# Performance work log

Hardware: AMD Instinct MI355X
Metric: run time of the kernel (lower is better)

The kernel has to match this reference:

```python
import jax, jax.numpy as jnp
import numpy as np

B, S, HID = 2, 2048, 4096
NH, NKV, HD = 32, 8, 128
G = 128  # quant group size along input dim
NEG_INF = -1e9


def _rope_tables(key):
    inv_freq = 1.0 / (10000.0 ** (jnp.arange(0, HD, 2, dtype=jnp.float32) / HD))  # [HD/2]
    pos = jnp.arange(S, dtype=jnp.float32)
    ang = pos[:, None] * inv_freq[None, :]                  # [S, HD/2]
    emb = jnp.concatenate([ang, ang], axis=-1)              # [S, HD]
    cos = jnp.broadcast_to(jnp.cos(emb)[None], (B, S, HD))
    sin = jnp.broadcast_to(jnp.sin(emb)[None], (B, S, HD))
    return cos, sin


def setup_inputs() -> dict:
    key = jax.random.key(0)
    ks = jax.random.split(key, 10)
    hidden_states = jax.random.normal(ks[0], (B, S, HID), dtype=jnp.float32)
    cos, sin = _rope_tables(ks[1])
    causal = jnp.tril(jnp.ones((S, S), dtype=bool))
    attention_mask = jnp.broadcast_to(
        jnp.where(causal, 0.0, NEG_INF).astype(jnp.float32)[None, None], (B, 1, S, S))

    def qlinear(k, out_dim, in_dim):
        k1, k2 = jax.random.split(k)
        qw = jax.random.randint(k1, (out_dim, in_dim), 0, 16, dtype=jnp.int32)
        scale = jax.random.uniform(k2, (out_dim, in_dim // G), dtype=jnp.float32) * 0.01 + 0.001
        return qw, scale

    q_qw, q_scale = qlinear(ks[2], NH * HD, HID)
    k_qw, k_scale = qlinear(ks[3], NKV * HD, HID)
    v_qw, v_scale = qlinear(ks[4], NKV * HD, HID)
    o_qw, o_scale = qlinear(ks[5], HID, NH * HD)
    return dict(hidden_states=hidden_states, cos=cos, sin=sin,
                attention_mask=attention_mask,
                q_qw=q_qw, q_scale=q_scale, k_qw=k_qw, k_scale=k_scale,
                v_qw=v_qw, v_scale=v_scale, o_qw=o_qw, o_scale=o_scale)


def _dequant(qw, scale):
    # int4 codes in [0,16), zero-point 8, per-(row, input-group) scale
    out_dim, in_dim = qw.shape
    w = (qw.astype(jnp.float32) - 8.0).reshape(out_dim, in_dim // G, G)
    return (w * scale[:, :, None]).reshape(out_dim, in_dim)


def _rotate_half(x):
    x1, x2 = jnp.split(x, 2, axis=-1)
    return jnp.concatenate([-x2, x1], axis=-1)


def reference(hidden_states, cos, sin, attention_mask,
              q_qw, q_scale, k_qw, k_scale, v_qw, v_scale, o_qw, o_scale):
    scaling = HD ** -0.5
    Wq = _dequant(q_qw, q_scale)
    Wk = _dequant(k_qw, k_scale)
    Wv = _dequant(v_qw, v_scale)
    Wo = _dequant(o_qw, o_scale)

    q = jnp.einsum('bsh,oh->bso', hidden_states, Wq).reshape(B, S, NH, HD).transpose(0, 2, 1, 3)
    k = jnp.einsum('bsh,oh->bso', hidden_states, Wk).reshape(B, S, NKV, HD).transpose(0, 2, 1, 3)
    v = jnp.einsum('bsh,oh->bso', hidden_states, Wv).reshape(B, S, NKV, HD).transpose(0, 2, 1, 3)

    c = cos[:, None, :, :]  # [B,1,S,HD]
    s = sin[:, None, :, :]
    q = q * c + _rotate_half(q) * s
    k = k * c + _rotate_half(k) * s

    groups = NH // NKV
    k = jnp.repeat(k, groups, axis=1)  # [B,NH,S,HD]
    v = jnp.repeat(v, groups, axis=1)

    scores = jnp.einsum('bhsd,bhtd->bhst', q, k) * scaling + attention_mask
    probs = jax.nn.softmax(scores, axis=-1)
    ctx = jnp.einsum('bhst,bhtd->bhsd', probs, v)        # [B,NH,S,HD]
    ctx = ctx.transpose(0, 2, 1, 3).reshape(B, S, NH * HD)
    return jnp.einsum('bso,ho->bsh', ctx, Wo.T) if False else jnp.einsum('bsi,oi->bso', ctx, Wo)
```

## Files before the change

### kernel.cpp

```cpp
#include <hip/hip_runtime.h>
#include <hip/hip_bf16.h>

#define B_ 2
#define S_ 2048
#define HID_ 4096
#define NH_ 32
#define NKV_ 8
#define HD_ 128
#define T_ (B_*S_)

typedef __bf16 bf16;
typedef __bf16 bf16x8 __attribute__((ext_vector_type(8)));
typedef __bf16 bf16x4 __attribute__((ext_vector_type(4)));
typedef float f32x4 __attribute__((ext_vector_type(4)));

__device__ __forceinline__ void load_lds16(const void* g, void* l) {
  __builtin_amdgcn_global_load_lds((const __attribute__((address_space(1))) void*)g,
                                   (__attribute__((address_space(3))) void*)l, 16, 0, 0);
}

#define DPP_ROR(x, n) __int_as_float(__builtin_amdgcn_update_dpp( \
    __float_as_int(x), __float_as_int(x), 0x120 | (n), 0xf, 0xf, false))
__device__ __forceinline__ float red16_max(float x) {
  x = fmaxf(x, DPP_ROR(x, 1)); x = fmaxf(x, DPP_ROR(x, 2));
  x = fmaxf(x, DPP_ROR(x, 4)); x = fmaxf(x, DPP_ROR(x, 8));
  return x;
}
__device__ __forceinline__ float red16_sum(float x) {
  x += DPP_ROR(x, 1); x += DPP_ROR(x, 2);
  x += DPP_ROR(x, 4); x += DPP_ROR(x, 8);
  return x;
}

__global__ __launch_bounds__(256) void cvt_bf16_kernel(const float* __restrict__ in,
                                                       bf16* __restrict__ out, int n4) {
  int idx = blockIdx.x * 256 + threadIdx.x;
  if (idx >= n4) return;
  float4 v = ((const float4*)in)[idx];
  bf16x4 o;
  o.x = (bf16)v.x; o.y = (bf16)v.y; o.z = (bf16)v.z; o.w = (bf16)v.w;
  ((bf16x4*)out)[idx] = o;
}

__global__ __launch_bounds__(256) void dequant_kernel(const int* __restrict__ qw,
                                                      const float* __restrict__ scale,
                                                      bf16* __restrict__ out,
                                                      int OD, int ID) {
  int idx = blockIdx.x * 256 + threadIdx.x;
  int perRow = ID >> 3;
  int total = OD * perRow;
  if (idx >= total) return;
  int o = idx / perRow;
  int ic = idx - o * perRow;
  float s = scale[o * (ID >> 7) + ((ic * 8) >> 7)];
  const int* q = qw + (size_t)o * ID + ic * 8;
  int4 q0 = *(const int4*)q;
  int4 q1 = *(const int4*)(q + 4);
  bf16x8 r;
  r[0] = (bf16)((q0.x - 8) * s);
  r[1] = (bf16)((q0.y - 8) * s);
  r[2] = (bf16)((q0.z - 8) * s);
  r[3] = (bf16)((q0.w - 8) * s);
  r[4] = (bf16)((q1.x - 8) * s);
  r[5] = (bf16)((q1.y - 8) * s);
  r[6] = (bf16)((q1.z - 8) * s);
  r[7] = (bf16)((q1.w - 8) * s);
  *(bf16x8*)(out + (size_t)o * ID + ic * 8) = r;
}

__global__ __launch_bounds__(256) void gemm_bt_kernel(const bf16* __restrict__ A,
                                                      const bf16* __restrict__ Bm,
                                                      void* __restrict__ Cout,
                                                      int N, int K, int c_fp32) {
  __shared__ bf16 As[8192];
  __shared__ bf16 Bs[8192];
  int tid = threadIdx.x;
  int wave = tid >> 6, lane = tid & 63, quad = lane >> 4, l16 = lane & 15;
  int m0 = blockIdx.y * 128, n0 = blockIdx.x * 128;
  int wm = (wave >> 1) * 64, wn = (wave & 1) * 64;

  int srow = lane >> 3;
  int schunk = (lane & 7) ^ (srow & 7);
  const bf16* Ab[4];
  const bf16* Bb[4];
#pragma unroll
  for (int u = 0; u < 4; u++) {
    int t = wave + 4 * u;
    Ab[u] = A  + (size_t)(m0 + 8 * t + srow) * K + schunk * 8;
    Bb[u] = Bm + (size_t)(n0 + 8 * t + srow) * K + schunk * 8;
  }

  f32x4 acc[4][4];
#pragma unroll
  for (int mt = 0; mt < 4; mt++)
#pragma unroll
    for (int nt = 0; nt < 4; nt++) acc[mt][nt] = (f32x4){0.f, 0.f, 0.f, 0.f};

  for (int k0 = 0; k0 < K; k0 += 64) {
    __syncthreads();
#pragma unroll
    for (int u = 0; u < 4; u++) {
      int t = wave + 4 * u;
      load_lds16(Ab[u] + k0, (char*)As + t * 1024);
      load_lds16(Bb[u] + k0, (char*)Bs + t * 1024);
    }
    __syncthreads();
#pragma unroll
    for (int kk = 0; kk < 2; kk++) {
      bf16x8 af[4], bfr[4];
#pragma unroll
      for (int mt = 0; mt < 4; mt++) {
        int r = wm + mt * 16 + l16;
        af[mt] = *(const bf16x8*)((const char*)As + r * 128 + (((kk * 4 + quad) ^ (r & 7)) << 4));
      }
#pragma unroll
      for (int nt = 0; nt < 4; nt++) {
        int r = wn + nt * 16 + l16;
        bfr[nt] = *(const bf16x8*)((const char*)Bs + r * 128 + (((kk * 4 + quad) ^ (r & 7)) << 4));
      }
#pragma unroll
      for (int mt = 0; mt < 4; mt++)
#pragma unroll
        for (int nt = 0; nt < 4; nt++)
          acc[mt][nt] = __builtin_amdgcn_mfma_f32_16x16x32_bf16(af[mt], bfr[nt], acc[mt][nt], 0, 0, 0);
    }
  }

#pragma unroll
  for (int mt = 0; mt < 4; mt++)
#pragma unroll
    for (int nt = 0; nt < 4; nt++)
#pragma unroll
      for (int r = 0; r < 4; r++) {
        int rr = m0 + wm + mt * 16 + quad * 4 + r;
        int cc = n0 + wn + nt * 16 + l16;
        if (c_fp32) ((float*)Cout)[(size_t)rr * N + cc] = acc[mt][nt][r];
        else        ((bf16*)Cout)[(size_t)rr * N + cc] = (bf16)acc[mt][nt][r];
      }
}

__global__ __launch_bounds__(256) void gemm_rope_kernel(const bf16* __restrict__ A,
                                                        const bf16* __restrict__ Bm,
                                                        bf16* __restrict__ Out,
                                                        int N, int K,
                                                        const float* __restrict__ cosT,
                                                        const float* __restrict__ sinT,
                                                        float outscale) {
  __shared__ char smem[32768];
  bf16* As = (bf16*)smem;
  bf16* Bs = (bf16*)(smem + 16384);
  float* Ex = (float*)smem;
  int tid = threadIdx.x;
  int wave = tid >> 6, lane = tid & 63, quad = lane >> 4, l16 = lane & 15;
  int m0 = blockIdx.y * 128, n0 = blockIdx.x * 128;
  int wm = (wave >> 1) * 64, wn = (wave & 1) * 64;

  int srow = lane >> 3;
  int schunk = (lane & 7) ^ (srow & 7);
  const bf16* Ab[4];
  const bf16* Bb[4];
#pragma unroll
  for (int u = 0; u < 4; u++) {
    int t = wave + 4 * u;
    Ab[u] = A  + (size_t)(m0 + 8 * t + srow) * K + schunk * 8;
    Bb[u] = Bm + (size_t)(n0 + 8 * t + srow) * K + schunk * 8;
  }

  f32x4 acc[4][4];
#pragma unroll
  for (int mt = 0; mt < 4; mt++)
#pragma unroll
    for (int nt = 0; nt < 4; nt++) acc[mt][nt] = (f32x4){0.f, 0.f, 0.f, 0.f};

  for (int k0 = 0; k0 < K; k0 += 64) {
    __syncthreads();
#pragma unroll
    for (int u = 0; u < 4; u++) {
      int t = wave + 4 * u;
      load_lds16(Ab[u] + k0, (char*)As + t * 1024);
      load_lds16(Bb[u] + k0, (char*)Bs + t * 1024);
    }
    __syncthreads();
#pragma unroll
    for (int kk = 0; kk < 2; kk++) {
      bf16x8 af[4], bfr[4];
#pragma unroll
      for (int mt = 0; mt < 4; mt++) {
        int r = wm + mt * 16 + l16;
        af[mt] = *(const bf16x8*)((const char*)As + r * 128 + (((kk * 4 + quad) ^ (r & 7)) << 4));
      }
#pragma unroll
      for (int nt = 0; nt < 4; nt++) {
        int r = wn + nt * 16 + l16;
        bfr[nt] = *(const bf16x8*)((const char*)Bs + r * 128 + (((kk * 4 + quad) ^ (r & 7)) << 4));
      }
#pragma unroll
      for (int mt = 0; mt < 4; mt++)
#pragma unroll
        for (int nt = 0; nt < 4; nt++)
          acc[mt][nt] = __builtin_amdgcn_mfma_f32_16x16x32_bf16(af[mt], bfr[nt], acc[mt][nt], 0, 0, 0);
    }
  }

  int myb = tid * 17;
  int pb = (tid ^ 64) * 17;
#pragma unroll
  for (int mt = 0; mt < 4; mt++) {
    __syncthreads();
#pragma unroll
    for (int nt = 0; nt < 4; nt++)
#pragma unroll
      for (int r = 0; r < 4; r++)
        Ex[myb + nt * 4 + r] = acc[mt][nt][r];
    __syncthreads();
    int rowb = m0 + wm + mt * 16 + quad * 4;
#pragma unroll
    for (int nt = 0; nt < 4; nt++) {
      int cc = n0 + wn + nt * 16 + l16;
      int d = cc & 127;
#pragma unroll
      for (int r = 0; r < 4; r++) {
        int row = rowb + r;
        int t = row & (S_ - 1);
        float self = acc[mt][nt][r];
        float other = Ex[pb + nt * 4 + r];
        float c = cosT[t * 128 + d], s = sinT[t * 128 + d];
        float o = (d < 64) ? (self * c - other * s) : (self * c + other * s);
        Out[(size_t)row * N + cc] = (bf16)(o * outscale);
      }
    }
  }
}

template<int FUSE_ROPE, int C_FP32>
__global__ __launch_bounds__(512, 2) void gemm256_kernel(const bf16* __restrict__ A,
                                                         const bf16* __restrict__ Bm,
                                                         void* __restrict__ Cout,
                                                         int N, int K,
                                                         const float* __restrict__ cosT,
                                                         const float* __restrict__ sinT,
                                                         float outscale) {
  __shared__ char smem[131072];
  const int tid = threadIdx.x;
  const int wave = tid >> 6, lane = tid & 63, quad = lane >> 4, l16 = lane & 15;
  const int wm = (wave >> 2) * 128, wn = (wave & 3) * 64;

  int bid = blockIdx.y * gridDim.x + blockIdx.x;
  int cpx = (gridDim.x * gridDim.y) >> 3;
  int wgid = (bid & 7) * cpx + (bid >> 3);
  int m0 = (wgid / gridDim.x) * 256;
  int n0 = (wgid % gridDim.x) * 256;

  const int srow = wave * 16 + (lane >> 2);
  const int sc = (lane & 3) ^ ((lane >> 2) & 3) ^ quad;
  const bf16* aS0 = A  + (size_t)(m0 + srow) * K + sc * 8;
  const bf16* aS1 = A  + (size_t)(m0 + 128 + srow) * K + sc * 8;
  const bf16* bS0 = Bm + (size_t)(n0 + srow) * K + sc * 8;
  const bf16* bS1 = Bm + (size_t)(n0 + 128 + srow) * K + sc * 8;
  const int wl = wave * 1024;

  const int rslot = ((quad ^ (l16 & 3) ^ ((l16 >> 2) & 3)) << 4);
  const int aoff = (wm + l16) * 64 + rslot;
  const int boff = (wn + l16) * 64 + rslot;

  f32x4 acc[8][4];
#pragma unroll
  for (int mt = 0; mt < 8; mt++)
#pragma unroll
    for (int nt = 0; nt < 4; nt++) acc[mt][nt] = (f32x4){0.f, 0.f, 0.f, 0.f};

  load_lds16(aS0,      smem +     0 + wl); load_lds16(aS1,      smem +  8192 + wl);
  load_lds16(bS0,      smem + 32768 + wl); load_lds16(bS1,      smem + 40960 + wl);
  load_lds16(aS0 + 32, smem + 16384 + wl); load_lds16(aS1 + 32, smem + 24576 + wl);
  load_lds16(bS0 + 32, smem + 49152 + wl); load_lds16(bS1 + 32, smem + 57344 + wl);
  asm volatile("s_waitcnt vmcnt(0)" ::: "memory");
  __builtin_amdgcn_s_barrier();

  const int NT = K >> 6;
  for (int t = 0; t < NT; ++t) {
    const char* base = smem + (t & 1) * 65536;
    char* nb = smem + ((t & 1) ^ 1) * 65536;
    const int off = (t + 1) << 6;
    const bool more = (t + 1) < NT;
    bf16x8 afA[4], afB[4], bfr[4];

#pragma unroll
    for (int i = 0; i < 4; i++) afA[i] = *(const bf16x8*)(base + aoff + i * 1024);
#pragma unroll
    for (int i = 0; i < 4; i++) bfr[i] = *(const bf16x8*)(base + 32768 + boff + i * 1024);
    if (more) { load_lds16(aS0 + off, nb + wl); load_lds16(aS1 + off, nb + 8192 + wl); }
    __builtin_amdgcn_s_barrier();
    __builtin_amdgcn_s_setprio(1);
#pragma unroll
    for (int mt = 0; mt < 4; mt++)
#pragma unroll
      for (int nt = 0; nt < 4; nt++)
        acc[mt][nt] = __builtin_amdgcn_mfma_f32_16x16x32_bf16(afA[mt], bfr[nt], acc[mt][nt], 0, 0, 0);
    __builtin_amdgcn_s_setprio(0);
    __builtin_amdgcn_s_barrier();

#pragma unroll
    for (int i = 0; i < 4; i++) afB[i] = *(const bf16x8*)(base + aoff + (i + 4) * 1024);
    if (more) { load_lds16(bS0 + off, nb + 32768 + wl); load_lds16(bS1 + off, nb + 40960 + wl); }
    if (t == NT - 1) asm volatile("s_waitcnt vmcnt(0)" ::: "memory");
    else             asm volatile("s_waitcnt vmcnt(4)" ::: "memory");
    __builtin_amdgcn_s_barrier();
    __builtin_amdgcn_s_setprio(1);
#pragma unroll
    for (int mt = 0; mt < 4; mt++)
#pragma unroll
      for (int nt = 0; nt < 4; nt++)
        acc[mt + 4][nt] = __builtin_amdgcn_mfma_f32_16x16x32_bf16(afB[mt], bfr[nt], acc[mt + 4][nt], 0, 0, 0);
    __builtin_amdgcn_s_setprio(0);
    __builtin_amdgcn_s_barrier();

#pragma unroll
    for (int i = 0; i < 4; i++) afA[i] = *(const bf16x8*)(base + 16384 + aoff + i * 1024);
#pragma unroll
    for (int i = 0; i < 4; i++) bfr[i] = *(const bf16x8*)(base + 49152 + boff + i * 1024);
    if (more) { load_lds16(aS0 + off + 32, nb + 16384 + wl); load_lds16(aS1 + off + 32, nb + 24576 + wl); }
    __builtin_amdgcn_s_barrier();
    __builtin_amdgcn_s_setprio(1);
#pragma unroll
    for (int mt = 0; mt < 4; mt++)
#pragma unroll
      for (int nt = 0; nt < 4; nt++)
        acc[mt][nt] = __builtin_amdgcn_mfma_f32_16x16x32_bf16(afA[mt], bfr[nt], acc[mt][nt], 0, 0, 0);
    __builtin_amdgcn_s_setprio(0);
    __builtin_amdgcn_s_barrier();

#pragma unroll
    for (int i = 0; i < 4; i++) afB[i] = *(const bf16x8*)(base + 16384 + aoff + (i + 4) * 1024);
    if (more) {
      load_lds16(bS0 + off + 32, nb + 49152 + wl); load_lds16(bS1 + off + 32, nb + 57344 + wl);
      asm volatile("s_waitcnt vmcnt(4)" ::: "memory");
    }
    __builtin_amdgcn_s_barrier();
    __builtin_amdgcn_s_setprio(1);
#pragma unroll
    for (int mt = 0; mt < 4; mt++)
#pragma unroll
      for (int nt = 0; nt < 4; nt++)
        acc[mt + 4][nt] = __builtin_amdgcn_mfma_f32_16x16x32_bf16(afB[mt], bfr[nt], acc[mt + 4][nt], 0, 0, 0);
    __builtin_amdgcn_s_setprio(0);
    __builtin_amdgcn_s_barrier();
  }

  if (FUSE_ROPE) {
    float* Ex = (float*)smem;
    int myb = tid * 17;
    int pb = (tid ^ 64) * 17;
#pragma unroll
    for (int mt = 0; mt < 8; mt++) {
      __syncthreads();
#pragma unroll
      for (int nt = 0; nt < 4; nt++)
#pragma unroll
        for (int r = 0; r < 4; r++)
          Ex[myb + nt * 4 + r] = acc[mt][nt][r];
      __syncthreads();
      int rowb = m0 + wm + mt * 16 + quad * 4;
#pragma unroll
      for (int nt = 0; nt < 4; nt++) {
        int cc = n0 + wn + nt * 16 + l16;
        int d = cc & 127;
#pragma unroll
        for (int r = 0; r < 4; r++) {
          int row = rowb + r;
          int tp = row & (S_ - 1);
          float self = acc[mt][nt][r];
          float other = Ex[pb + nt * 4 + r];
          float c = cosT[tp * 128 + d], s = sinT[tp * 128 + d];
          float o = (d < 64) ? (self * c - other * s) : (self * c + other * s);
          ((bf16*)Cout)[(size_t)row * N + cc] = (bf16)(o * outscale);
        }
      }
    }
  } else {
#pragma unroll
    for (int mt = 0; mt < 8; mt++)
#pragma unroll
      for (int nt = 0; nt < 4; nt++)
#pragma unroll
        for (int r = 0; r < 4; r++) {
          int rr = m0 + wm + mt * 16 + quad * 4 + r;
          int cc = n0 + wn + nt * 16 + l16;
          if (C_FP32) ((float*)Cout)[(size_t)rr * N + cc] = acc[mt][nt][r];
          else        ((bf16*)Cout)[(size_t)rr * N + cc] = (bf16)acc[mt][nt][r];
        }
  }
}

__global__ __launch_bounds__(512, 4) void attn_kernel(const bf16* __restrict__ Qm,
                                                      const bf16* __restrict__ Km,
                                                      const bf16* __restrict__ VtG,
                                                      bf16* __restrict__ Cm) {
  __shared__ char sK[32768];
  __shared__ char sV[16384];
  __shared__ char sP[16384];
  int tid = threadIdx.x;
  int wave = tid >> 6, lane = tid & 63, quad = lane >> 4, l16 = lane & 15;
  int h = blockIdx.y, b = blockIdx.z;
  int kvh = h >> 2;

  const bf16* Kb[2];
  const bf16* Vb[2];
  {
    int r4 = lane >> 4, c16 = lane & 15;
    int r8 = lane >> 3, c8 = lane & 7;
#pragma unroll
    for (int u = 0; u < 2; u++) {
      int t = wave * 2 + u;
      int key = 4 * t + r4;
      int kc = c16 ^ (key & 7);
      Kb[u] = Km + (size_t)(b * S_ + key) * (NKV_ * HD_) + kvh * HD_ + kc * 8;
      int d = 8 * t + r8;
      int vc = c8 ^ (d & 7);
      Vb[u] = VtG + (size_t)(kvh * HD_ + d) * T_ + (size_t)b * S_ + vc * 8;
    }
  }

  for (int pass = 0; pass < 2; pass++) {
    int qt = pass ? ((S_ / 128 - 1) - (int)blockIdx.x) : (int)blockIdx.x;
    int q0 = qt * 128;
    int jend = q0 + 128;

#pragma unroll
    for (int u = 0; u < 2; u++)
      load_lds16(Kb[u], sK + (wave * 2 + u) * 1024);

    bf16x8 aQ[4];
    {
      int row = q0 + wave * 16 + l16;
      const bf16* qb = Qm + (size_t)(b * S_ + row) * (NH_ * HD_) + h * HD_;
#pragma unroll
      for (int kt = 0; kt < 4; kt++)
        aQ[kt] = *(const bf16x8*)(qb + kt * 32 + quad * 8);
    }

    float mcur[4], lcur[4];
    f32x4 O[8];
#pragma unroll
    for (int r = 0; r < 4; r++) { mcur[r] = -1e30f; lcur[r] = 0.f; }
#pragma unroll
    for (int n = 0; n < 8; n++) O[n] = (f32x4){0.f, 0.f, 0.f, 0.f};

    for (int j0 = 0; j0 < jend; j0 += 64) {
      int cur = (j0 >> 6) & 1;
      __syncthreads();
      if (j0 + 64 < jend) {
#pragma unroll
        for (int u = 0; u < 2; u++)
          load_lds16(Kb[u] + (size_t)(j0 + 64) * (NKV_ * HD_),
                     sK + (1 - cur) * 16384 + (wave * 2 + u) * 1024);
      }
#pragma unroll
      for (int u = 0; u < 2; u++)
        load_lds16(Vb[u] + j0, sV + (wave * 2 + u) * 1024);

      const char* Kc = sK + cur * 16384;
      f32x4 sc[4];
#pragma unroll
      for (int nt = 0; nt < 4; nt++) sc[nt] = (f32x4){0.f, 0.f, 0.f, 0.f};
#pragma unroll
      for (int kt = 0; kt < 4; kt++) {
        bf16x8 bk[4];
#pragma unroll
        for (int nt = 0; nt < 4; nt++) {
          int key = nt * 16 + l16;
          bk[nt] = *(const bf16x8*)(Kc + key * 256 + (((kt * 4 + quad) ^ (key & 7)) << 4));
        }
#pragma unroll
        for (int nt = 0; nt < 4; nt++)
          sc[nt] = __builtin_amdgcn_mfma_f32_16x16x32_bf16(aQ[kt], bk[nt], sc[nt], 0, 0, 0);
      }

      int rowb = q0 + wave * 16 + quad * 4;
      if (j0 + 63 > q0 + wave * 16) {
#pragma unroll
        for (int nt = 0; nt < 4; nt++) {
          int col = j0 + nt * 16 + l16;
#pragma unroll
          for (int r = 0; r < 4; r++)
            if (col > rowb + r) sc[nt][r] = -1e9f;
        }
      }

      float rmax[4], alpha[4], rsum[4];
#pragma unroll
      for (int r = 0; r < 4; r++) {
        float v = fmaxf(fmaxf(sc[0][r], sc[1][r]), fmaxf(sc[2][r], sc[3][r]));
        rmax[r] = red16_max(v);
        float mnew = fmaxf(mcur[r], rmax[r]);
        alpha[r] = exp2f(mcur[r] - mnew);
        mcur[r] = mnew;
      }
#pragma unroll
      for (int nt = 0; nt < 4; nt++)
#pragma unroll
        for (int r = 0; r < 4; r++)
          sc[nt][r] = exp2f(sc[nt][r] - mcur[r]);
#pragma unroll
      for (int r = 0; r < 4; r++) {
        float s = (sc[0][r] + sc[1][r]) + (sc[2][r] + sc[3][r]);
        rsum[r] = red16_sum(s);
        lcur[r] = lcur[r] * alpha[r] + rsum[r];
      }
#pragma unroll
      for (int n = 0; n < 8; n++)
#pragma unroll
        for (int r = 0; r < 4; r++) O[n][r] *= alpha[r];

      char* Pw = sP + wave * 2048;
#pragma unroll
      for (int nt = 0; nt < 4; nt++) {
        int key = nt * 16 + l16;
#pragma unroll
        for (int r = 0; r < 4; r++) {
          int m = quad * 4 + r;
          *(bf16*)(Pw + m * 128 + (((key >> 3) ^ (m & 7)) << 4) + (key & 7) * 2) =
              (bf16)sc[nt][r];
        }
      }

      __syncthreads();

#pragma unroll
      for (int kt = 0; kt < 2; kt++) {
        bf16x8 ap = *(const bf16x8*)(Pw + l16 * 128 + (((kt * 4 + quad) ^ (l16 & 7)) << 4));
#pragma unroll
        for (int nt = 0; nt < 8; nt++) {
          int d = nt * 16 + l16;
          bf16x8 bv = *(const bf16x8*)(sV + d * 128 + (((kt * 4 + quad) ^ (d & 7)) << 4));
          O[nt] = __builtin_amdgcn_mfma_f32_16x16x32_bf16(ap, bv, O[nt], 0, 0, 0);
        }
      }
    }

#pragma unroll
    for (int nt = 0; nt < 8; nt++)
#pragma unroll
      for (int r = 0; r < 4; r++) {
        int row = q0 + wave * 16 + quad * 4 + r;
        Cm[(size_t)(b * S_ + row) * (NH_ * HD_) + h * HD_ + nt * 16 + l16] =
            (bf16)(O[nt][r] / lcur[r]);
      }
  }
}

extern "C" void kernel_launch(void* const* d_in, const int* in_sizes, int n_in,
                              void* d_out, int out_size, void* d_ws, size_t ws_size,
                              hipStream_t stream) {
  const float* hidden = (const float*)d_in[0];
  const float* cosT   = (const float*)d_in[1];
  const float* sinT   = (const float*)d_in[2];
  const int*   q_qw = (const int*)d_in[4];
  const float* q_sc = (const float*)d_in[5];
  const int*   k_qw = (const int*)d_in[6];
  const float* k_sc = (const float*)d_in[7];
  const int*   v_qw = (const int*)d_in[8];
  const float* v_sc = (const float*)d_in[9];
  const int*   o_qw = (const int*)d_in[10];
  const float* o_sc = (const float*)d_in[11];

  const size_t MB = 1024 * 1024;
  char* ws = (char*)d_ws;
  bf16* Xb  = (bf16*)(ws);
  bf16* Wb  = (bf16*)(ws + 32 * MB);
  bf16* Qm  = (bf16*)(ws + 64 * MB);
  bf16* Km  = (bf16*)(ws + 96 * MB);
  bf16* VtG = (bf16*)(ws + 104 * MB);
  bf16* Cm  = Xb;

  cvt_bf16_kernel<<<(T_ * HID_ / 4 + 255) / 256, 256, 0, stream>>>(hidden, Xb, T_ * HID_ / 4);

  const float qscale = (float)(0.08838834764831845 * 1.4426950408889634);

  dequant_kernel<<<(4096 * 512 + 255) / 256, 256, 0, stream>>>(q_qw, q_sc, Wb, 4096, 4096);
  gemm256_kernel<1, 0><<<dim3(16, 16), 512, 0, stream>>>(Xb, Wb, Qm, 4096, 4096,
                                                         cosT, sinT, qscale);

  dequant_kernel<<<(1024 * 512 + 255) / 256, 256, 0, stream>>>(k_qw, k_sc, Wb, 1024, 4096);
  gemm_rope_kernel<<<dim3(8, 32), 256, 0, stream>>>(Xb, Wb, Km, 1024, 4096, cosT, sinT, 1.0f);

  dequant_kernel<<<(1024 * 512 + 255) / 256, 256, 0, stream>>>(v_qw, v_sc, Wb, 1024, 4096);
  gemm_bt_kernel<<<dim3(32, 8), 256, 0, stream>>>(Wb, Xb, VtG, 4096, 4096, 0);

  attn_kernel<<<dim3(8, NH_, B_), 512, 0, stream>>>(Qm, Km, VtG, Cm);

  dequant_kernel<<<(4096 * 512 + 255) / 256, 256, 0, stream>>>(o_qw, o_sc, Wb, 4096, 4096);
  gemm256_kernel<0, 1><<<dim3(16, 16), 512, 0, stream>>>(Cm, Wb, d_out, 4096, 4096,
                                                         nullptr, nullptr, 1.0f);
}
```

Measured before the change: 829.1 us.

## Skip fully masked attention tiles per wave and lazily rescale softmax

In the flash-attention loop, each wave now skips QK and PV MFMA work for key tiles that are entirely above the causal diagonal for its 16 rows. The online softmax only rescales O and the running sum when some row's max exceeds the stored max by more than a threshold, checked wave-wide. Row sums are kept per lane and reduced once at the end, and the final divide becomes a reciprocal multiply. The P tile's LDS swizzle is changed to depend on the quad. Lazy rescaling lets exp2 arguments reach about 8 above the stored max, which bounds intermediate values but adds some precision risk.

```diff
diff --git a/kernel.cpp b/kernel.cpp
--- a/kernel.cpp
+++ b/kernel.cpp
@@ -438,10 +438,10 @@
         aQ[kt] = *(const bf16x8*)(qb + kt * 32 + quad * 8);
     }
 
-    float mcur[4], lcur[4];
+    float mcur[4], psum[4];
     f32x4 O[8];
 #pragma unroll
-    for (int r = 0; r < 4; r++) { mcur[r] = -1e30f; lcur[r] = 0.f; }
+    for (int r = 0; r < 4; r++) { mcur[r] = -1e30f; psum[r] = 0.f; }
 #pragma unroll
     for (int n = 0; n < 8; n++) O[n] = (f32x4){0.f, 0.f, 0.f, 0.f};
 
@@ -458,92 +458,109 @@
       for (int u = 0; u < 2; u++)
         load_lds16(Vb[u] + j0, sV + (wave * 2 + u) * 1024);
 
-      const char* Kc = sK + cur * 16384;
-      f32x4 sc[4];
-#pragma unroll
-      for (int nt = 0; nt < 4; nt++) sc[nt] = (f32x4){0.f, 0.f, 0.f, 0.f};
-#pragma unroll
-      for (int kt = 0; kt < 4; kt++) {
-        bf16x8 bk[4];
+      bool active = (j0 <= q0 + wave * 16 + 15);
+
+      if (active) {
+        const char* Kc = sK + cur * 16384;
+        f32x4 sc[4];
+#pragma unroll
+        for (int nt = 0; nt < 4; nt++) sc[nt] = (f32x4){0.f, 0.f, 0.f, 0.f};
+#pragma unroll
+        for (int kt = 0; kt < 4; kt++) {
+          bf16x8 bk[4];
+#pragma unroll
+          for (int nt = 0; nt < 4; nt++) {
+            int key = nt * 16 + l16;
+            bk[nt] = *(const bf16x8*)(Kc + key * 256 + (((kt * 4 + quad) ^ (key & 7)) << 4));
+          }
+#pragma unroll
+          for (int nt = 0; nt < 4; nt++)
+            sc[nt] = __builtin_amdgcn_mfma_f32_16x16x32_bf16(aQ[kt], bk[nt], sc[nt], 0, 0, 0);
+        }
+
+        int rowb = q0 + wave * 16 + quad * 4;
+        if (j0 + 63 > q0 + wave * 16) {
+#pragma unroll
+          for (int nt = 0; nt < 4; nt++) {
+            int col = j0 + nt * 16 + l16;
+#pragma unroll
+            for (int r = 0; r < 4; r++)
+              if (col > rowb + r) sc[nt][r] = -1e9f;
+          }
+        }
+
+        float vmax[4];
+#pragma unroll
+        for (int r = 0; r < 4; r++)
+          vmax[r] = fmaxf(fmaxf(sc[0][r], sc[1][r]), fmaxf(sc[2][r], sc[3][r]));
+        int nd = 0;
+#pragma unroll
+        for (int r = 0; r < 4; r++) nd |= (vmax[r] > mcur[r] + 8.f) ? 1 : 0;
+        if (__any(nd)) {
+          float al[4];
+#pragma unroll
+          for (int r = 0; r < 4; r++) {
+            float rm = red16_max(vmax[r]);
+            float mnew = fmaxf(mcur[r], rm);
+            al[r] = exp2f(mcur[r] - mnew);
+            mcur[r] = mnew;
+            psum[r] *= al[r];
+          }
+#pragma unroll
+          for (int n = 0; n < 8; n++)
+#pragma unroll
+            for (int r = 0; r < 4; r++) O[n][r] *= al[r];
+        }
+#pragma unroll
+        for (int nt = 0; nt < 4; nt++)
+#pragma unroll
+          for (int r = 0; r < 4; r++)
+            sc[nt][r] = exp2f(sc[nt][r] - mcur[r]);
+#pragma unroll
+        for (int r = 0; r < 4; r++)
+          psum[r] += (sc[0][r] + sc[1][r]) + (sc[2][r] + sc[3][r]);
+
+        char* Pw = sP + wave * 2048;
 #pragma unroll
         for (int nt = 0; nt < 4; nt++) {
           int key = nt * 16 + l16;
-          bk[nt] = *(const bf16x8*)(Kc + key * 256 + (((kt * 4 + quad) ^ (key & 7)) << 4));
+#pragma unroll
+          for (int r = 0; r < 4; r++) {
+            int m = quad * 4 + r;
+            *(bf16*)(Pw + m * 128 + ((((key >> 3) ^ (2 * quad)) & 7) << 4) + (key & 7) * 2) =
+                (bf16)sc[nt][r];
+          }
         }
-#pragma unroll
-        for (int nt = 0; nt < 4; nt++)
-          sc[nt] = __builtin_amdgcn_mfma_f32_16x16x32_bf16(aQ[kt], bk[nt], sc[nt], 0, 0, 0);
-      }
-
-      int rowb = q0 + wave * 16 + quad * 4;
-      if (j0 + 63 > q0 + wave * 16) {
-#pragma unroll
-        for (int nt = 0; nt < 4; nt++) {
-          int col = j0 + nt * 16 + l16;
-#pragma unroll
-          for (int r = 0; r < 4; r++)
-            if (col > rowb + r) sc[nt][r] = -1e9f;
+      }
+
+      __syncthreads();
+
+      if (active) {
+        char* Pw = sP + wave * 2048;
+#pragma unroll
+        for (int kt = 0; kt < 2; kt++) {
+          bf16x8 ap = *(const bf16x8*)(Pw + l16 * 128 +
+                      ((((kt * 4 + quad) ^ (2 * ((l16 >> 2) & 3))) & 7) << 4));
+#pragma unroll
+          for (int nt = 0; nt < 8; nt++) {
+            int d = nt * 16 + l16;
+            bf16x8 bv = *(const bf16x8*)(sV + d * 128 + (((kt * 4 + quad) ^ (d & 7)) << 4));
+            O[nt] = __builtin_amdgcn_mfma_f32_16x16x32_bf16(ap, bv, O[nt], 0, 0, 0);
+          }
         }
       }
-
-      float rmax[4], alpha[4], rsum[4];
-#pragma unroll
-      for (int r = 0; r < 4; r++) {
-        float v = fmaxf(fmaxf(sc[0][r], sc[1][r]), fmaxf(sc[2][r], sc[3][r]));
-        rmax[r] = red16_max(v);
-        float mnew = fmaxf(mcur[r], rmax[r]);
-        alpha[r] = exp2f(mcur[r] - mnew);
-        mcur[r] = mnew;
-      }
-#pragma unroll
-      for (int nt = 0; nt < 4; nt++)
-#pragma unroll
-        for (int r = 0; r < 4; r++)
-          sc[nt][r] = exp2f(sc[nt][r] - mcur[r]);
-#pragma unroll
-      for (int r = 0; r < 4; r++) {
-        float s = (sc[0][r] + sc[1][r]) + (sc[2][r] + sc[3][r]);
-        rsum[r] = red16_sum(s);
-        lcur[r] = lcur[r] * alpha[r] + rsum[r];
-      }
-#pragma unroll
-      for (int n = 0; n < 8; n++)
-#pragma unroll
-        for (int r = 0; r < 4; r++) O[n][r] *= alpha[r];
-
-      char* Pw = sP + wave * 2048;
-#pragma unroll
-      for (int nt = 0; nt < 4; nt++) {
-        int key = nt * 16 + l16;
-#pragma unroll
-        for (int r = 0; r < 4; r++) {
-          int m = quad * 4 + r;
-          *(bf16*)(Pw + m * 128 + (((key >> 3) ^ (m & 7)) << 4) + (key & 7) * 2) =
-              (bf16)sc[nt][r];
-        }
-      }
-
-      __syncthreads();
-
-#pragma unroll
-      for (int kt = 0; kt < 2; kt++) {
-        bf16x8 ap = *(const bf16x8*)(Pw + l16 * 128 + (((kt * 4 + quad) ^ (l16 & 7)) << 4));
-#pragma unroll
-        for (int nt = 0; nt < 8; nt++) {
-          int d = nt * 16 + l16;
-          bf16x8 bv = *(const bf16x8*)(sV + d * 128 + (((kt * 4 + quad) ^ (d & 7)) << 4));
-          O[nt] = __builtin_amdgcn_mfma_f32_16x16x32_bf16(ap, bv, O[nt], 0, 0, 0);
-        }
-      }
-    }
-
+    }
+
+    float linv[4];
+#pragma unroll
+    for (int r = 0; r < 4; r++) linv[r] = 1.0f / red16_sum(psum[r]);
 #pragma unroll
     for (int nt = 0; nt < 8; nt++)
 #pragma unroll
       for (int r = 0; r < 4; r++) {
         int row = q0 + wave * 16 + quad * 4 + r;
         Cm[(size_t)(b * S_ + row) * (NH_ * HD_) + h * HD_ + nt * 16 + l16] =
-            (bf16)(O[nt][r] / lcur[r]);
+            (bf16)(O[nt][r] * linv[r]);
       }
   }
 }
```

Result: faster. 800.4 us (-3.5%).
